# Kernel tuning notes

Hardware: AMD Instinct MI355X
Metric: run time of the kernel (lower is better)

The kernel has to match this reference:

```python
import jax, jax.numpy as jnp
import numpy as np

HEADS = 8
DIM_HEAD = 64
SCALE = DIM_HEAD ** -0.5
EPS = 1e-12  # F.normalize default eps


def setup_inputs() -> dict:
    key = jax.random.key(0)
    ks = jax.random.split(key, 4)
    B, C, H, W = 16, 256, 64, 64
    hidden = HEADS * DIM_HEAD  # 512
    x = jax.random.normal(ks[0], (B, C, H, W), dtype=jnp.float32)
    w_qkv = jax.random.normal(ks[1], (3 * hidden, C), dtype=jnp.float32) * (C ** -0.5)
    w_out = jax.random.normal(ks[2], (C, hidden), dtype=jnp.float32) * (hidden ** -0.5)
    b_out = jax.random.normal(ks[3], (C,), dtype=jnp.float32) * 0.01
    g = jnp.ones((1, C, 1, 1), dtype=jnp.float32)
    return {"x": x, "w_qkv": w_qkv, "w_out": w_out, "b_out": b_out, "g": g}


def reference(x, w_qkv, w_out, b_out, g):
    B, C, H, W = x.shape
    N = H * W
    hidden = HEADS * DIM_HEAD
    # 1x1 conv == channel matmul: [B, 3*hidden, N]
    qkv = jnp.einsum('oc,bcn->bon', w_qkv, x.reshape(B, C, N))
    qkv = qkv.reshape(B, 3, HEADS, DIM_HEAD, N)
    q, k, v = qkv[:, 0], qkv[:, 1], qkv[:, 2]  # each [B, h, d, N]
    q = jax.nn.softmax(q, axis=2) * SCALE      # softmax over channel dim d
    k = jax.nn.softmax(k, axis=3)              # softmax over spatial dim n
    context = jnp.einsum('bhdn,bhen->bhde', k, v)   # [B, h, d, e]
    out = jnp.einsum('bhde,bhdn->bhen', context, q) # [B, h, e, N]
    out = out.reshape(B, hidden, N)
    # to_out: 1x1 conv with bias
    y = jnp.einsum('oc,bcn->bon', w_out, out) + b_out[None, :, None]
    y = y.reshape(B, C, H, W)
    # RMSNorm: F.normalize over channel dim, * g * sqrt(W) (x.shape[-1] == width)
    norm = jnp.sqrt(jnp.sum(y * y, axis=1, keepdims=True))
    y = y / jnp.maximum(norm, EPS)
    return y * g * (W ** 0.5)
```

## Files before the change

### kernel.cpp

```cpp
#include <hip/hip_runtime.h>
#include <hip/hip_bf16.h>

#define NPIX 4096
#define CIN  256
#define HID  512
#define QROWS 1536
#define NB   16

typedef unsigned int u32;
typedef unsigned short u16;
typedef float f32x4 __attribute__((ext_vector_type(4)));
typedef short bf16x8 __attribute__((ext_vector_type(8)));

__device__ __forceinline__ float bf2f(u16 u){
  union { u32 i; float f; } v; v.i = ((u32)u) << 16; return v.f;
}
__device__ __forceinline__ u16 f2bf(float f){
  union { float f; u32 u; } v; v.f = f;
  u32 r = v.u + 0x7fffu + ((v.u >> 16) & 1u);
  return (u16)(r >> 16);
}
__device__ __forceinline__ u32 pkbf(float a, float b){
  __hip_bfloat162 h = __float22bfloat162_rn(make_float2(a, b));
  union { __hip_bfloat162 h; u32 u; } cv; cv.h = h; return cv.u;
}
__device__ __forceinline__ void gload16(const u16* g, u16* l){
  __builtin_amdgcn_global_load_lds(
      (const __attribute__((address_space(1))) void*)g,
      (__attribute__((address_space(3))) void*)l, 16, 0, 0);
}

__device__ __forceinline__ float waveRedMax(float v){
  #pragma unroll
  for (int o = 32; o > 0; o >>= 1) v = fmaxf(v, __shfl_xor(v, o, 64));
  return v;
}
__device__ __forceinline__ float waveRedSum(float v){
  #pragma unroll
  for (int o = 32; o > 0; o >>= 1) v += __shfl_xor(v, o, 64);
  return v;
}

__global__ void k_marker(float* y, int n){
  int i = blockIdx.x * 256 + threadIdx.x;
  if (i < n) y[i] = 1.0e6f;
}

__global__ __launch_bounds__(256) void k_cvt(const float* __restrict__ src,
                                             u16* __restrict__ dst){
  const int i = (blockIdx.x * 256 + threadIdx.x) * 8;
  const float4 a = *(const float4*)(src + i);
  const float4 b = *(const float4*)(src + i + 4);
  *(uint4*)(dst + i) = make_uint4(pkbf(a.x,a.y), pkbf(a.z,a.w),
                                  pkbf(b.x,b.y), pkbf(b.z,b.w));
}

__global__ __launch_bounds__(256) void k_xt(const float* __restrict__ X,
                                            u16* __restrict__ Xt){
  __shared__ float ls[64][67];
  const int n0 = blockIdx.x * 64, c0 = blockIdx.y * 64, b = blockIdx.z;
  const int tid = threadIdx.x;
  const float* Xb = X + (size_t)b * CIN * NPIX;

  {
    const int r = tid >> 2, cq = (tid & 3) * 16;
    #pragma unroll
    for (int j = 0; j < 4; ++j)
      *(float4*)&ls[r][cq + j*4] = *(const float4*)&Xb[(size_t)(c0 + r) * NPIX + n0 + cq + j*4];
  }
  __syncthreads();
  {
    const int nr = tid >> 2, cs = (tid & 3) * 16;
    u32 pk[8];
    #pragma unroll
    for (int j = 0; j < 8; ++j)
      pk[j] = pkbf(ls[cs + 2*j][nr], ls[cs + 2*j + 1][nr]);
    u16* dst = Xt + (size_t)b * NPIX * CIN + (size_t)(n0 + nr) * CIN + c0 + cs;
    *(uint4*)(dst)     = make_uint4(pk[0], pk[1], pk[2], pk[3]);
    *(uint4*)(dst + 8) = make_uint4(pk[4], pk[5], pk[6], pk[7]);
  }
}

__global__ __launch_bounds__(256, 3) void k_qkv(
    const u16* __restrict__ Wq, const u16* __restrict__ Xt, u16* __restrict__ QKV)
{
  __shared__ __align__(16) u16 pool[17408];
  u16* As = pool;
  u16* Bs = pool + 8192;

  const int flat = blockIdx.x;
  const int virt = (flat & 7) * 768 + (flat >> 3);
  const int o0 = (virt % 12) * 128;
  const int n0 = ((virt / 12) & 31) * 128;
  const int b  = virt / 384;

  const int tid = threadIdx.x;
  const int lane = tid & 63;
  const int wv = tid >> 6;
  const int wr = wv >> 1, wc = wv & 1;
  const int g  = lane >> 4;
  const int c  = lane & 15;
  const u16* Xb = Xt + (size_t)b * NPIX * CIN;

  const int grow = lane >> 3;
  const int gch  = (lane & 7) * 8;

  f32x4 acc[4][4];
  #pragma unroll
  for (int i = 0; i < 4; ++i)
    #pragma unroll
    for (int j = 0; j < 4; ++j) acc[i][j] = (f32x4){0.f, 0.f, 0.f, 0.f};

  for (int s = 0; s < 4; ++s) {
    const int k0 = s * 64;
    #pragma unroll
    for (int i = 0; i < 4; ++i) {
      const int j = wv * 4 + i;
      const int row = j * 8 + grow;
      gload16(&Xb[(size_t)(n0 + row) * CIN + k0 + gch], &As[j * 512]);
      gload16(&Wq[(size_t)(o0 + row) * CIN + k0 + gch], &Bs[j * 512]);
    }
    __syncthreads();

    #pragma unroll
    for (int ks = 0; ks < 2; ++ks) {
      bf16x8 af[4], bfr[4];
      #pragma unroll
      for (int mf = 0; mf < 4; ++mf)
        af[mf] = *(const bf16x8*)&As[(wr * 64 + mf * 16 + c) * 64 + ks * 32 + g * 8];
      #pragma unroll
      for (int nf = 0; nf < 4; ++nf)
        bfr[nf] = *(const bf16x8*)&Bs[(wc * 64 + nf * 16 + c) * 64 + ks * 32 + g * 8];
      #pragma unroll
      for (int mf = 0; mf < 4; ++mf)
        #pragma unroll
        for (int nf = 0; nf < 4; ++nf)
          acc[mf][nf] = __builtin_amdgcn_mfma_f32_16x16x32_bf16(
              af[mf], bfr[nf], acc[mf][nf], 0, 0, 0);
    }
    __syncthreads();
  }

  #pragma unroll
  for (int mf = 0; mf < 4; ++mf) {
    const int nrow = wr * 64 + mf * 16 + g * 4;
    #pragma unroll
    for (int nf = 0; nf < 4; ++nf) {
      const int ocol = wc * 64 + nf * 16 + c;
      #pragma unroll
      for (int r = 0; r < 4; ++r)
        pool[ocol * 136 + nrow + r] = f2bf(acc[mf][nf][r]);
    }
  }
  __syncthreads();
  u16* dst = QKV + (size_t)b * QROWS * NPIX;
  #pragma unroll
  for (int i = 0; i < 8; ++i) {
    const int f2 = i * 256 + tid;
    const int orow = f2 >> 4, ch = f2 & 15;
    const uint4 v = *(const uint4*)&pool[orow * 136 + ch * 8];
    *(uint4*)&dst[(size_t)(o0 + orow) * NPIX + n0 + ch * 8] = v;
  }
}

__global__ __launch_bounds__(256) void k_kstats(const u16* __restrict__ QKV,
                                                float2* __restrict__ stats)
{
  __shared__ float sred[4];
  __shared__ float sbc;
  const int r = blockIdx.x;
  const int b = r >> 9, hd = r & 511;
  const u16* row = QKV + ((size_t)b * QROWS + HID + hd) * NPIX;
  const int tid = threadIdx.x;
  const int wv = tid >> 6, ln = tid & 63;

  float vals[16];
  float mx = -3.0e38f;
  #pragma unroll
  for (int rep = 0; rep < 2; ++rep) {
    const uint4 raw = *(const uint4*)(row + (rep*256 + tid)*8);
    const u32 w[4] = {raw.x, raw.y, raw.z, raw.w};
    #pragma unroll
    for (int j = 0; j < 4; ++j){
      const float f0 = bf2f((u16)(w[j] & 0xffff));
      const float f1 = bf2f((u16)(w[j] >> 16));
      vals[rep*8 + 2*j]     = f0;
      vals[rep*8 + 2*j + 1] = f1;
      mx = fmaxf(mx, fmaxf(f0, f1));
    }
  }
  mx = waveRedMax(mx);
  if (ln == 0) sred[wv] = mx;
  __syncthreads();
  if (tid == 0) sbc = fmaxf(fmaxf(sred[0],sred[1]), fmaxf(sred[2],sred[3]));
  __syncthreads();
  const float M = sbc;
  float s = 0.f;
  #pragma unroll
  for (int i = 0; i < 16; ++i) s += __expf(vals[i] - M);
  s = waveRedSum(s);
  __syncthreads();
  if (ln == 0) sred[wv] = s;
  __syncthreads();
  if (tid == 0) stats[r] = make_float2(M, sred[0]+sred[1]+sred[2]+sred[3]);
}

__global__ __launch_bounds__(256) void k_ctx(const u16* __restrict__ QKV,
    const float2* __restrict__ stats, float* __restrict__ ctxp)
{
  __shared__ __align__(16) u16 ks[64 * 72];
  __shared__ __align__(16) u16 vs[64 * 72];
  __shared__ float smx[64], sinv[64];
  const int split = blockIdx.x, h = blockIdx.y, b = blockIdx.z;
  const int tid = threadIdx.x;
  const int lane = tid & 63, wv = tid >> 6;
  const int g = lane >> 4, c = lane & 15;
  if (tid < 64) {
    const float2 st = stats[b * HID + h * 64 + tid];
    smx[tid]  = st.x;
    sinv[tid] = 1.0f / st.y;
  }
  __syncthreads();
  const u16* kb = QKV + ((size_t)b * QROWS + HID     + h * 64) * NPIX;
  const u16* vb = QKV + ((size_t)b * QROWS + 2 * HID + h * 64) * NPIX;

  const int srow = tid >> 2;
  const int sch  = (tid & 3) * 16;
  const float sm = smx[srow], siv = sinv[srow];

  f32x4 acc[4];
  #pragma unroll
  for (int j = 0; j < 4; ++j) acc[j] = (f32x4){0.f, 0.f, 0.f, 0.f};

  for (int t = 0; t < 16; ++t) {
    const int n0 = split * 1024 + t * 64;
    {
      const uint4 r0 = *(const uint4*)(kb + (size_t)srow * NPIX + n0 + sch);
      const uint4 r1 = *(const uint4*)(kb + (size_t)srow * NPIX + n0 + sch + 8);
      const u32 w[8] = {r0.x, r0.y, r0.z, r0.w, r1.x, r1.y, r1.z, r1.w};
      u32 pk[8];
      #pragma unroll
      for (int j = 0; j < 8; ++j) {
        const float lo = __expf(bf2f((u16)(w[j] & 0xffff)) - sm) * siv;
        const float hi = __expf(bf2f((u16)(w[j] >> 16))    - sm) * siv;
        pk[j] = pkbf(lo, hi);
      }
      *(uint4*)&ks[srow * 72 + sch]     = make_uint4(pk[0], pk[1], pk[2], pk[3]);
      *(uint4*)&ks[srow * 72 + sch + 8] = make_uint4(pk[4], pk[5], pk[6], pk[7]);
      const uint4 v0 = *(const uint4*)(vb + (size_t)srow * NPIX + n0 + sch);
      const uint4 v1 = *(const uint4*)(vb + (size_t)srow * NPIX + n0 + sch + 8);
      *(uint4*)&vs[srow * 72 + sch]     = v0;
      *(uint4*)&vs[srow * 72 + sch + 8] = v1;
    }
    __syncthreads();
    #pragma unroll
    for (int ks2 = 0; ks2 < 2; ++ks2) {
      const bf16x8 af = *(const bf16x8*)&ks[(wv * 16 + c) * 72 + ks2 * 32 + g * 8];
      #pragma unroll
      for (int nf = 0; nf < 4; ++nf) {
        const bf16x8 bf = *(const bf16x8*)&vs[(nf * 16 + c) * 72 + ks2 * 32 + g * 8];
        acc[nf] = __builtin_amdgcn_mfma_f32_16x16x32_bf16(af, bf, acc[nf], 0, 0, 0);
      }
    }
    __syncthreads();
  }
  float* dst = ctxp + (size_t)split * (NB*8*64*64) + ((size_t)(b*8+h)) * 4096;
  #pragma unroll
  for (int nf = 0; nf < 4; ++nf)
    #pragma unroll
    for (int r = 0; r < 4; ++r)
      dst[(wv*16 + g*4 + r) * 64 + nf*16 + c] = acc[nf][r];
}

__global__ __launch_bounds__(256) void k_ctxred(const float* __restrict__ ctxp,
                                                float* __restrict__ ctx)
{
  const int SZ = NB*8*64*64;
  const int i = (blockIdx.x * 256 + threadIdx.x) * 4;
  float4 a  = *(const float4*)(ctxp + i);
  const float4 c1 = *(const float4*)(ctxp + SZ   + i);
  const float4 c2 = *(const float4*)(ctxp + 2*SZ + i);
  const float4 c3 = *(const float4*)(ctxp + 3*SZ + i);
  a.x += c1.x + c2.x + c3.x;
  a.y += c1.y + c2.y + c3.y;
  a.z += c1.z + c2.z + c3.z;
  a.w += c1.w + c2.w + c3.w;
  *(float4*)(ctx + i) = a;
}

__global__ __launch_bounds__(256) void k_qctx(u16* __restrict__ QKV,
    const float* __restrict__ ctx)
{
  __shared__ __align__(16) u16 As[256 * 72];
  __shared__ __align__(16) u16 Bs[64 * 72];
  const int nt = blockIdx.x, h = blockIdx.y, b = blockIdx.z;
  const int n0 = nt * 256;
  const int tid = threadIdx.x;
  const int lane = tid & 63, wv = tid >> 6;
  const int g = lane >> 4, c = lane & 15;

  const float* cbase = ctx + ((size_t)(b*8+h)) * 4096;
  #pragma unroll
  for (int j = 0; j < 16; ++j) {
    const int idx = tid + j * 256;
    const int d = idx >> 6, e = idx & 63;
    Bs[e * 72 + d] = f2bf(cbase[idx]);
  }

  const u16* qb = QKV + ((size_t)b*QROWS + h*64) * NPIX;
  float vals[64];
  float mx = -3.0e38f;
  #pragma unroll
  for (int d = 0; d < 64; ++d) {
    vals[d] = bf2f(qb[(size_t)d * NPIX + n0 + tid]);
    mx = fmaxf(mx, vals[d]);
  }
  float s = 0.f;
  #pragma unroll
  for (int d = 0; d < 64; ++d) { vals[d] = __expf(vals[d] - mx); s += vals[d]; }
  const float sc = 0.125f / s;
  #pragma unroll
  for (int q = 0; q < 8; ++q) {
    u32 pk[4];
    #pragma unroll
    for (int p = 0; p < 4; ++p)
      pk[p] = pkbf(vals[q*8 + 2*p] * sc, vals[q*8 + 2*p + 1] * sc);
    *(uint4*)&As[tid * 72 + q * 8] = make_uint4(pk[0], pk[1], pk[2], pk[3]);
  }
  __syncthreads();

  f32x4 acc[4][4];
  #pragma unroll
  for (int i = 0; i < 4; ++i)
    #pragma unroll
    for (int j = 0; j < 4; ++j) acc[i][j] = (f32x4){0.f, 0.f, 0.f, 0.f};
  #pragma unroll
  for (int ks = 0; ks < 2; ++ks) {
    bf16x8 af[4], bfr[4];
    #pragma unroll
    for (int mf = 0; mf < 4; ++mf)
      af[mf] = *(const bf16x8*)&As[(wv * 64 + mf * 16 + c) * 72 + ks * 32 + g * 8];
    #pragma unroll
    for (int nf = 0; nf < 4; ++nf)
      bfr[nf] = *(const bf16x8*)&Bs[(nf * 16 + c) * 72 + ks * 32 + g * 8];
    #pragma unroll
    for (int mf = 0; mf < 4; ++mf)
      #pragma unroll
      for (int nf = 0; nf < 4; ++nf)
        acc[mf][nf] = __builtin_amdgcn_mfma_f32_16x16x32_bf16(
            af[mf], bfr[nf], acc[mf][nf], 0, 0, 0);
  }
  __syncthreads();

  u16* pool = As;
  #pragma unroll
  for (int mf = 0; mf < 4; ++mf) {
    const int nrow = wv * 64 + mf * 16 + g * 4;
    #pragma unroll
    for (int nf = 0; nf < 4; ++nf) {
      const int ecol = nf * 16 + c;
      #pragma unroll
      for (int r = 0; r < 4; ++r)
        pool[ecol * 264 + nrow + r] = f2bf(acc[mf][nf][r]);
    }
  }
  __syncthreads();
  u16* ob = QKV + ((size_t)b*QROWS + h*64) * NPIX;
  #pragma unroll
  for (int i = 0; i < 8; ++i) {
    const int f2 = i * 256 + tid;
    const int erow = f2 >> 5, ch = f2 & 31;
    const uint4 v = *(const uint4*)&pool[erow * 264 + ch * 8];
    *(uint4*)&ob[(size_t)erow * NPIX + n0 + ch * 8] = v;
  }
}

__global__ __launch_bounds__(256) void k_proj(const u16* __restrict__ QKV,
    const u16* __restrict__ Wbf, const float* __restrict__ bo,
    const float* __restrict__ gg, float* __restrict__ Y)
{
  __shared__ __align__(16) u16 As[256][72];
  __shared__ __align__(16) u16 Bs[64][72];
  __shared__ float red[4][64];
  __shared__ float sbias[256], sgain[256];
  const int nt = blockIdx.x, b = blockIdx.y;
  const int n0 = nt * 64;
  const int tid = threadIdx.x;
  const int lane = tid & 63, wv = tid >> 6;
  const int g = lane >> 4, c = lane & 15;
  const u16* ob = QKV + (size_t)b * QROWS * NPIX;

  sbias[tid] = bo[tid];
  sgain[tid] = gg[tid];

  f32x4 acc[4][4];
  #pragma unroll
  for (int i = 0; i < 4; ++i)
    #pragma unroll
    for (int j = 0; j < 4; ++j) acc[i][j] = (f32x4){0.f, 0.f, 0.f, 0.f};

  for (int s = 0; s < 8; ++s) {
    const int k0 = s * 64;
    #pragma unroll
    for (int i = 0; i < 8; ++i) {
      const int flat = i * 256 + tid;
      const int row = flat >> 3, kc = flat & 7;
      *(uint4*)&As[row][kc * 8] =
          *(const uint4*)&Wbf[(size_t)row * HID + k0 + kc * 8];
    }
    {
      const int kb0 = wv * 16;
      u16 vals[16];
      #pragma unroll
      for (int kk = 0; kk < 16; ++kk)
        vals[kk] = ob[(size_t)(k0 + kb0 + kk) * NPIX + n0 + lane];
      u32 pk[8];
      #pragma unroll
      for (int j = 0; j < 8; ++j)
        pk[j] = (u32)vals[2*j] | ((u32)vals[2*j+1] << 16);
      *(uint4*)&Bs[lane][kb0]     = make_uint4(pk[0], pk[1], pk[2], pk[3]);
      *(uint4*)&Bs[lane][kb0 + 8] = make_uint4(pk[4], pk[5], pk[6], pk[7]);
    }
    __syncthreads();

    #pragma unroll
    for (int ks = 0; ks < 2; ++ks) {
      bf16x8 af[4], bfr[4];
      #pragma unroll
      for (int mf = 0; mf < 4; ++mf)
        af[mf] = *(const bf16x8*)&As[wv * 64 + mf * 16 + c][ks * 32 + g * 8];
      #pragma unroll
      for (int nf = 0; nf < 4; ++nf)
        bfr[nf] = *(const bf16x8*)&Bs[nf * 16 + c][ks * 32 + g * 8];
      #pragma unroll
      for (int mf = 0; mf < 4; ++mf)
        #pragma unroll
        for (int nf = 0; nf < 4; ++nf)
          acc[mf][nf] = __builtin_amdgcn_mfma_f32_16x16x32_bf16(
              af[mf], bfr[nf], acc[mf][nf], 0, 0, 0);
    }
    __syncthreads();
  }

  #pragma unroll
  for (int mf = 0; mf < 4; ++mf)
    #pragma unroll
    for (int r = 0; r < 4; ++r) {
      const float bb = sbias[wv * 64 + mf * 16 + g * 4 + r];
      #pragma unroll
      for (int nf = 0; nf < 4; ++nf) acc[mf][nf][r] += bb;
    }

  #pragma unroll
  for (int nf = 0; nf < 4; ++nf) {
    float v = 0.f;
    #pragma unroll
    for (int mf = 0; mf < 4; ++mf)
      #pragma unroll
      for (int r = 0; r < 4; ++r)
        v = fmaf(acc[mf][nf][r], acc[mf][nf][r], v);
    v += __shfl_xor(v, 16, 64);
    v += __shfl_xor(v, 32, 64);
    if (g == 0) red[wv][nf * 16 + c] = v;
  }
  __syncthreads();
  float scale[4];
  #pragma unroll
  for (int nf = 0; nf < 4; ++nf) {
    const int col = nf * 16 + c;
    const float tot = red[0][col] + red[1][col] + red[2][col] + red[3][col];
    scale[nf] = 8.0f / fmaxf(sqrtf(tot), 1e-12f);
  }

  float* yb = Y + (size_t)b * CIN * NPIX;
  #pragma unroll
  for (int mf = 0; mf < 4; ++mf)
    #pragma unroll
    for (int r = 0; r < 4; ++r) {
      const int row = wv * 64 + mf * 16 + g * 4 + r;
      const float gr = sgain[row];
      #pragma unroll
      for (int nf = 0; nf < 4; ++nf)
        yb[(size_t)row * NPIX + n0 + nf * 16 + c] = acc[mf][nf][r] * scale[nf] * gr;
    }
}

extern "C" void kernel_launch(void* const* d_in, const int* in_sizes, int n_in,
                              void* d_out, int out_size, void* d_ws, size_t ws_size,
                              hipStream_t stream) {
  const float* x     = (const float*)d_in[0];
  const float* w_qkv = (const float*)d_in[1];
  const float* w_out = (const float*)d_in[2];
  const float* b_out = (const float*)d_in[3];
  const float* g     = (const float*)d_in[4];
  float* y = (float*)d_out;

  char* ws = (char*)d_ws;
  u16*    qkv   = (u16*)(ws);
  u16*    xt    = (u16*)(ws + 201326592);
  float2* stats = (float2*)(ws + 201326592);
  float*  ctx   = (float*)(ws + 201392128);
  float*  ctxp  = (float*)(ws + 203489280);
  u16*    wbf   = (u16*)(ws + 234881024);
  u16*    wqb   = (u16*)(ws + 235143168);

  if (ws_size < 235929600) {
    k_marker<<<dim3((out_size + 255) / 256), 256, 0, stream>>>(y, out_size);
    return;
  }

  k_cvt   <<<dim3(64),         256, 0, stream>>>(w_out, wbf);
  k_cvt   <<<dim3(192),        256, 0, stream>>>(w_qkv, wqb);
  k_xt    <<<dim3(64, 4, 16),  256, 0, stream>>>(x, xt);
  k_qkv   <<<dim3(6144),       256, 0, stream>>>(wqb, xt, qkv);
  k_kstats<<<dim3(8192),       256, 0, stream>>>(qkv, stats);
  k_ctx   <<<dim3(4, 8, 16),   256, 0, stream>>>(qkv, stats, ctxp);
  k_ctxred<<<dim3(512),        256, 0, stream>>>(ctxp, ctx);
  k_qctx  <<<dim3(16, 8, 16),  256, 0, stream>>>(qkv, ctx);
  k_proj  <<<dim3(64, 16),     256, 0, stream>>>(qkv, wbf, b_out, g, y);
}
```

Before: 203.7 us.

## Fold key softmax normalization into context reduction, drop separate stats pass

Removes the k_kstats kernel, which read all of K to compute per-row max and sum. k_ctx now applies exp without max subtraction, accumulates partial row sums per split, and k_ctxred divides the reduced context by the total sum. This saves one full read of K and a kernel launch. The cost is losing the max-subtraction stability, so exp can overflow for large logits.

```diff
diff --git a/kernel.cpp b/kernel.cpp
--- a/kernel.cpp
+++ b/kernel.cpp
@@ -28,17 +28,6 @@
   __builtin_amdgcn_global_load_lds(
       (const __attribute__((address_space(1))) void*)g,
       (__attribute__((address_space(3))) void*)l, 16, 0, 0);
-}
-
-__device__ __forceinline__ float waveRedMax(float v){
-  #pragma unroll
-  for (int o = 32; o > 0; o >>= 1) v = fmaxf(v, __shfl_xor(v, o, 64));
-  return v;
-}
-__device__ __forceinline__ float waveRedSum(float v){
-  #pragma unroll
-  for (int o = 32; o > 0; o >>= 1) v += __shfl_xor(v, o, 64);
-  return v;
 }
 
 __global__ void k_marker(float* y, int n){
@@ -163,74 +152,25 @@
   }
 }
 
-__global__ __launch_bounds__(256) void k_kstats(const u16* __restrict__ QKV,
-                                                float2* __restrict__ stats)
-{
-  __shared__ float sred[4];
-  __shared__ float sbc;
-  const int r = blockIdx.x;
-  const int b = r >> 9, hd = r & 511;
-  const u16* row = QKV + ((size_t)b * QROWS + HID + hd) * NPIX;
-  const int tid = threadIdx.x;
-  const int wv = tid >> 6, ln = tid & 63;
-
-  float vals[16];
-  float mx = -3.0e38f;
-  #pragma unroll
-  for (int rep = 0; rep < 2; ++rep) {
-    const uint4 raw = *(const uint4*)(row + (rep*256 + tid)*8);
-    const u32 w[4] = {raw.x, raw.y, raw.z, raw.w};
-    #pragma unroll
-    for (int j = 0; j < 4; ++j){
-      const float f0 = bf2f((u16)(w[j] & 0xffff));
-      const float f1 = bf2f((u16)(w[j] >> 16));
-      vals[rep*8 + 2*j]     = f0;
-      vals[rep*8 + 2*j + 1] = f1;
-      mx = fmaxf(mx, fmaxf(f0, f1));
-    }
-  }
-  mx = waveRedMax(mx);
-  if (ln == 0) sred[wv] = mx;
-  __syncthreads();
-  if (tid == 0) sbc = fmaxf(fmaxf(sred[0],sred[1]), fmaxf(sred[2],sred[3]));
-  __syncthreads();
-  const float M = sbc;
-  float s = 0.f;
-  #pragma unroll
-  for (int i = 0; i < 16; ++i) s += __expf(vals[i] - M);
-  s = waveRedSum(s);
-  __syncthreads();
-  if (ln == 0) sred[wv] = s;
-  __syncthreads();
-  if (tid == 0) stats[r] = make_float2(M, sred[0]+sred[1]+sred[2]+sred[3]);
-}
-
 __global__ __launch_bounds__(256) void k_ctx(const u16* __restrict__ QKV,
-    const float2* __restrict__ stats, float* __restrict__ ctxp)
+    float* __restrict__ ctxp, float* __restrict__ Sp)
 {
   __shared__ __align__(16) u16 ks[64 * 72];
   __shared__ __align__(16) u16 vs[64 * 72];
-  __shared__ float smx[64], sinv[64];
   const int split = blockIdx.x, h = blockIdx.y, b = blockIdx.z;
   const int tid = threadIdx.x;
   const int lane = tid & 63, wv = tid >> 6;
   const int g = lane >> 4, c = lane & 15;
-  if (tid < 64) {
-    const float2 st = stats[b * HID + h * 64 + tid];
-    smx[tid]  = st.x;
-    sinv[tid] = 1.0f / st.y;
-  }
-  __syncthreads();
   const u16* kb = QKV + ((size_t)b * QROWS + HID     + h * 64) * NPIX;
   const u16* vb = QKV + ((size_t)b * QROWS + 2 * HID + h * 64) * NPIX;
 
   const int srow = tid >> 2;
   const int sch  = (tid & 3) * 16;
-  const float sm = smx[srow], siv = sinv[srow];
 
   f32x4 acc[4];
   #pragma unroll
   for (int j = 0; j < 4; ++j) acc[j] = (f32x4){0.f, 0.f, 0.f, 0.f};
+  float s_part = 0.f;
 
   for (int t = 0; t < 16; ++t) {
     const int n0 = split * 1024 + t * 64;
@@ -241,8 +181,9 @@
       u32 pk[8];
       #pragma unroll
       for (int j = 0; j < 8; ++j) {
-        const float lo = __expf(bf2f((u16)(w[j] & 0xffff)) - sm) * siv;
-        const float hi = __expf(bf2f((u16)(w[j] >> 16))    - sm) * siv;
+        const float lo = __expf(bf2f((u16)(w[j] & 0xffff)));
+        const float hi = __expf(bf2f((u16)(w[j] >> 16)));
+        s_part += lo + hi;
         pk[j] = pkbf(lo, hi);
       }
       *(uint4*)&ks[srow * 72 + sch]     = make_uint4(pk[0], pk[1], pk[2], pk[3]);
@@ -264,6 +205,11 @@
     }
     __syncthreads();
   }
+  s_part += __shfl_xor(s_part, 1, 64);
+  s_part += __shfl_xor(s_part, 2, 64);
+  if ((tid & 3) == 0)
+    Sp[(size_t)split * 8192 + (b * 8 + h) * 64 + srow] = s_part;
+
   float* dst = ctxp + (size_t)split * (NB*8*64*64) + ((size_t)(b*8+h)) * 4096;
   #pragma unroll
   for (int nf = 0; nf < 4; ++nf)
@@ -273,18 +219,23 @@
 }
 
 __global__ __launch_bounds__(256) void k_ctxred(const float* __restrict__ ctxp,
+                                                const float* __restrict__ Sp,
                                                 float* __restrict__ ctx)
 {
   const int SZ = NB*8*64*64;
   const int i = (blockIdx.x * 256 + threadIdx.x) * 4;
+  const int bh = i >> 12, d = (i >> 6) & 63;
+  const int si = bh * 64 + d;
+  const float S = Sp[si] + Sp[8192 + si] + Sp[16384 + si] + Sp[24576 + si];
+  const float inv = 1.0f / S;
   float4 a  = *(const float4*)(ctxp + i);
   const float4 c1 = *(const float4*)(ctxp + SZ   + i);
   const float4 c2 = *(const float4*)(ctxp + 2*SZ + i);
   const float4 c3 = *(const float4*)(ctxp + 3*SZ + i);
-  a.x += c1.x + c2.x + c3.x;
-  a.y += c1.y + c2.y + c3.y;
-  a.z += c1.z + c2.z + c3.z;
-  a.w += c1.w + c2.w + c3.w;
+  a.x = (a.x + c1.x + c2.x + c3.x) * inv;
+  a.y = (a.y + c1.y + c2.y + c3.y) * inv;
+  a.z = (a.z + c1.z + c2.z + c3.z) * inv;
+  a.w = (a.w + c1.w + c2.w + c3.w) * inv;
   *(float4*)(ctx + i) = a;
 }
 
@@ -498,9 +449,9 @@
   char* ws = (char*)d_ws;
   u16*    qkv   = (u16*)(ws);
   u16*    xt    = (u16*)(ws + 201326592);
-  float2* stats = (float2*)(ws + 201326592);
   float*  ctx   = (float*)(ws + 201392128);
   float*  ctxp  = (float*)(ws + 203489280);
+  float*  Sp    = (float*)(ws + 211877888);
   u16*    wbf   = (u16*)(ws + 234881024);
   u16*    wqb   = (u16*)(ws + 235143168);
 
@@ -513,9 +464,8 @@
   k_cvt   <<<dim3(192),        256, 0, stream>>>(w_qkv, wqb);
   k_xt    <<<dim3(64, 4, 16),  256, 0, stream>>>(x, xt);
   k_qkv   <<<dim3(6144),       256, 0, stream>>>(wqb, xt, qkv);
-  k_kstats<<<dim3(8192),       256, 0, stream>>>(qkv, stats);
-  k_ctx   <<<dim3(4, 8, 16),   256, 0, stream>>>(qkv, stats, ctxp);
-  k_ctxred<<<dim3(512),        256, 0, stream>>>(ctxp, ctx);
+  k_ctx   <<<dim3(4, 8, 16),   256, 0, stream>>>(qkv, ctxp, Sp);
+  k_ctxred<<<dim3(512),        256, 0, stream>>>(ctxp, Sp, ctx);
   k_qctx  <<<dim3(16, 8, 16),  256, 0, stream>>>(qkv, ctx);
   k_proj  <<<dim3(64, 16),     256, 0, stream>>>(qkv, wbf, b_out, g, y);
 }
```

After: 192.8 us. -5.4%, faster.
